# Optimization experiments

Hardware: AMD Instinct MI355X
Metric: run time of the kernel (lower is better)

## Reference

```python
import jax, jax.numpy as jnp
import numpy as np
from jax import lax

N, EMB, AED, H, KCL = 4096, 768, 512, 8, 32
HD = AED // H
TEMP, THR, EPS, MAX_IT = 0.5, 1e-4, 1e-6, 100


def setup_inputs() -> dict:
    key = jax.random.key(0)
    ks = jax.random.split(key, 9)
    s = 0.02
    return {
        "embeddings": jax.random.normal(ks[0], (N, EMB), jnp.float32),
        "qw": jax.random.normal(ks[1], (EMB, AED), jnp.float32) * s,
        "kw": jax.random.normal(ks[2], (EMB, AED), jnp.float32) * s,
        "vw": jax.random.normal(ks[3], (EMB, AED), jnp.float32) * s,
        "in_proj_w": jax.random.normal(ks[4], (3 * AED, AED), jnp.float32) * s,
        "in_proj_b": jnp.zeros((3 * AED,), jnp.float32),
        "out_w": jax.random.normal(ks[5], (AED, AED), jnp.float32) * s,
        "out_b": jnp.zeros((AED,), jnp.float32),
        "init_idx": jax.random.randint(ks[6], (KCL,), 0, N, dtype=jnp.int32),
    }


def _mha(q, k, v, Wi, bi, Wo, bo):
    # torch nn.MultiheadAttention, batch_first, batch==1, no mask
    Wq, Wk, Wv = jnp.split(Wi, 3, axis=0)
    bq, bk, bv = jnp.split(bi, 3)
    n = q.shape[0]
    qh = (q @ Wq.T + bq).reshape(n, H, HD).transpose(1, 0, 2)  # [H,N,hd]
    kh = (k @ Wk.T + bk).reshape(n, H, HD).transpose(1, 0, 2)
    vh = (v @ Wv.T + bv).reshape(n, H, HD).transpose(1, 0, 2)
    scores = jnp.einsum("hqd,hkd->hqk", qh, kh) / jnp.sqrt(jnp.float32(HD))
    attn = jax.nn.softmax(scores, axis=-1)            # [H,N,N]
    o = jnp.einsum("hqk,hkd->hqd", attn, vh)          # [H,N,hd]
    o = o.transpose(1, 0, 2).reshape(n, AED)
    return o @ Wo.T + bo


def _cdist(X, C):
    # euclidean distance [N,K]
    d2 = (jnp.sum(X * X, 1)[:, None] + jnp.sum(C * C, 1)[None, :]
          - 2.0 * (X @ C.T))
    return jnp.sqrt(jnp.maximum(d2, 0.0))


def _dkm_step(X, C):
    a = jax.nn.softmax(-_cdist(X, C) / TEMP, axis=1)  # [N,K]
    a_sum = jnp.sum(a, axis=0) + EPS                  # [K]
    C_new = (a.T @ X) / a_sum[:, None]                # [K,E]
    return a, C_new


def _dkm(X, C_init):
    a, C_new = _dkm_step(X, C_init)
    diff = jnp.sum(jnp.abs(C_new - C_init))
    def body(carry, _):
        C, a, C_new, diff = carry
        cont = diff > THR
        C2 = jnp.where(cont, C_new, C)
        a2, C_new2 = _dkm_step(X, C2)
        a2 = jnp.where(cont, a2, a)
        C_new2 = jnp.where(cont, C_new2, C_new)
        diff2 = jnp.where(cont, jnp.sum(jnp.abs(C_new2 - C2)), diff)
        return (C2, a2, C_new2, diff2), None
    (C, a, _, _), _ = lax.scan(body, (C_init, a, C_new, diff), None, length=MAX_IT)
    return C, a


def reference(embeddings, qw, kw, vw, in_proj_w, in_proj_b, out_w, out_b, init_idx):
    q = embeddings @ qw
    k = embeddings @ kw
    v = embeddings @ vw
    tr = _mha(q, k, v, in_proj_w, in_proj_b, out_w, out_b)  # [N,AED]
    init_c = lax.stop_gradient(tr[init_idx])                # detached init
    C, a = _dkm(tr, init_c)
    return C, a
```

## Files before the change

### kernel.cpp

```cpp
#include <hip/hip_runtime.h>
#include <hip/hip_bf16.h>


typedef __hip_bfloat16 bf16;
typedef __attribute__((ext_vector_type(8))) short s16x8;
typedef __attribute__((ext_vector_type(4))) float f32x4;

__device__ __forceinline__ void  stv(float* p, float v) { *p = v; }
__device__ __forceinline__ void  stv(bf16*  p, float v) { *p = __float2bfloat16(v); }

__device__ __forceinline__ float gload(const float* p)
{
    return __hip_atomic_load(p, __ATOMIC_RELAXED, __HIP_MEMORY_SCOPE_AGENT);
}
__device__ __forceinline__ void gstore(float* p, float v)
{
    __hip_atomic_store(p, v, __ATOMIC_RELAXED, __HIP_MEMORY_SCOPE_AGENT);
}
__device__ __forceinline__ void gstore2(float2* p, float2 v)
{
    unsigned long long u; __builtin_memcpy(&u, &v, 8);
    __hip_atomic_store((unsigned long long*)p, u, __ATOMIC_RELAXED, __HIP_MEMORY_SCOPE_AGENT);
}

__device__ __forceinline__ unsigned bf16word(float v)
{
    bf16 b = __float2bfloat16(v);
    unsigned short u;
    __builtin_memcpy(&u, &b, 2);
    return ((unsigned)u) << 16;
}

__device__ __forceinline__ void stage8(const float* g, bf16* d)
{
    const float4 a = *(const float4*)g;
    const float4 b = *(const float4*)(g + 4);
    union { uint4 u; bf16 h[8]; } r;
    r.h[0] = __float2bfloat16(a.x); r.h[1] = __float2bfloat16(a.y);
    r.h[2] = __float2bfloat16(a.z); r.h[3] = __float2bfloat16(a.w);
    r.h[4] = __float2bfloat16(b.x); r.h[5] = __float2bfloat16(b.y);
    r.h[6] = __float2bfloat16(b.z); r.h[7] = __float2bfloat16(b.w);
    *(uint4*)d = r.u;
}
__device__ __forceinline__ void stage8(const bf16* g, bf16* d)
{
    *(uint4*)d = *(const uint4*)g;
}
__device__ __forceinline__ void load8f(const float* g, float* v)
{
    const float4 a = *(const float4*)g; const float4 b = *(const float4*)(g + 4);
    v[0]=a.x; v[1]=a.y; v[2]=a.z; v[3]=a.w; v[4]=b.x; v[5]=b.y; v[6]=b.z; v[7]=b.w;
}
__device__ __forceinline__ void load8f(const bf16* g, float* v)
{
    union { uint4 u; bf16 h[8]; } r; r.u = *(const uint4*)g;
#pragma unroll
    for (int j = 0; j < 8; j++) v[j] = __bfloat162float(r.h[j]);
}

struct P3 { const void* a[3]; const void* b[3]; const float* bi[3]; void* c[3]; };

template<typename TA, typename TB, typename TC, bool BT, bool BIAS>
__global__ __launch_bounds__(256) void mgemm(P3 p, int M, int N, int K)
{
    __shared__ __align__(16) bf16 As[64][40];
    __shared__ __align__(16) bf16 Bs[64][40];
    const int z = blockIdx.z;
    const TA* A = (const TA*)p.a[z];
    const TB* B = (const TB*)p.b[z];
    const float* bias = p.bi[z];
    TC* C = (TC*)p.c[z];
    const int m0 = blockIdx.x * 64, n0 = blockIdx.y * 64;
    const int t = threadIdx.x;
    const int w = t >> 6, lane = t & 63, quad = lane >> 4, l15 = lane & 15;
    f32x4 acc[4];
#pragma unroll
    for (int i = 0; i < 4; i++) acc[i] = (f32x4){0.f, 0.f, 0.f, 0.f};
    for (int k0 = 0; k0 < K; k0 += 32) {
        {
            int r = t >> 2, c = (t & 3) * 8;
            stage8(&A[(size_t)(m0 + r) * K + k0 + c], &As[r][c]);
        }
        if constexpr (BT) {
            int r = t >> 2, c = (t & 3) * 8;
            stage8(&B[(size_t)(n0 + r) * K + k0 + c], &Bs[r][c]);
        } else {
            int k = t >> 3, n8 = (t & 7) * 8;
            float v[8];
            load8f(&B[(size_t)(k0 + k) * N + n0 + n8], v);
#pragma unroll
            for (int j = 0; j < 8; j++) Bs[n8 + j][k] = __float2bfloat16(v[j]);
        }
        __syncthreads();
        s16x8 af = *(const s16x8*)&As[w * 16 + l15][quad * 8];
#pragma unroll
        for (int nt = 0; nt < 4; nt++) {
            s16x8 bfv = *(const s16x8*)&Bs[nt * 16 + l15][quad * 8];
            acc[nt] = __builtin_amdgcn_mfma_f32_16x16x32_bf16(af, bfv, acc[nt], 0, 0, 0);
        }
        __syncthreads();
    }
#pragma unroll
    for (int nt = 0; nt < 4; nt++) {
        int col = n0 + nt * 16 + l15;
        float bv = 0.f;
        if constexpr (BIAS) bv = bias[col];
#pragma unroll
        for (int r = 0; r < 4; r++) {
            int row = m0 + w * 16 + quad * 4 + r;
            stv(&C[(size_t)row * N + col], acc[nt][r] + bv);
        }
    }
}

__global__ __launch_bounds__(256) void attn_mfma(
    const bf16* __restrict__ qh, const bf16* __restrict__ kh,
    const bf16* __restrict__ vh, bf16* __restrict__ oatt)
{
    __shared__ __align__(16) bf16  Qs[64][72];
    __shared__ __align__(16) bf16  Ks[2][64][72];
    __shared__ __align__(16) bf16  Vt[2][64][72];
    __shared__ __align__(16) float Ss[64][68];
    __shared__ __align__(16) bf16  Ps[64][72];
    __shared__ float mrow[64], lrow[64], arow[64];
    const int bid = blockIdx.x;
    const int h = bid & 7, q0 = (bid >> 3) * 64;
    const int t = threadIdx.x;
    const int w = t >> 6, lane = t & 63, quad = lane >> 4, l15 = lane & 15;

#pragma unroll
    for (int i = 0; i < 2; i++) {
        int idx = t + i * 256;
        int r = idx >> 3, c = (idx & 7) * 8;
        *(uint4*)&Qs[r][c] = *(const uint4*)&qh[(size_t)(q0 + r) * 512 + h * 64 + c];
    }
    if (t < 64) { mrow[t] = -1e30f; lrow[t] = 0.f; }
    f32x4 accO[4];
#pragma unroll
    for (int i = 0; i < 4; i++) accO[i] = (f32x4){0.f, 0.f, 0.f, 0.f};

    const int sidx0 = t, sidx1 = t + 256;
    const int sr0 = sidx0 >> 3, sc0 = (sidx0 & 7) * 8;
    const int sr1 = sidx1 >> 3, sc1v = (sidx1 & 7) * 8;
    uint4 kreg0 = *(const uint4*)&kh[(size_t)sr0 * 512 + h * 64 + sc0];
    uint4 vreg0 = *(const uint4*)&vh[(size_t)sr0 * 512 + h * 64 + sc0];
    uint4 kreg1 = *(const uint4*)&kh[(size_t)sr1 * 512 + h * 64 + sc1v];
    uint4 vreg1 = *(const uint4*)&vh[(size_t)sr1 * 512 + h * 64 + sc1v];
    {
        *(uint4*)&Ks[0][sr0][sc0] = kreg0;
        union { uint4 u; bf16 b[8]; } vv; vv.u = vreg0;
        int rlo = sr0 & 7, rch = sr0 >> 3, rx = sidx0 & 7;
#pragma unroll
        for (int j = 0; j < 8; j++)
            Vt[0][sc0 + j][rlo | (((rch ^ rx) & 7) << 3)] = vv.b[j];
    }
    {
        *(uint4*)&Ks[0][sr1][sc1v] = kreg1;
        union { uint4 u; bf16 b[8]; } vv; vv.u = vreg1;
        int rlo = sr1 & 7, rch = sr1 >> 3, rx = sidx1 & 7;
#pragma unroll
        for (int j = 0; j < 8; j++)
            Vt[0][sc1v + j][rlo | (((rch ^ rx) & 7) << 3)] = vv.b[j];
    }
    {
        size_t base0 = (size_t)(64 + sr0) * 512 + h * 64;
        size_t base1 = (size_t)(64 + sr1) * 512 + h * 64;
        kreg0 = *(const uint4*)&kh[base0 + sc0];
        vreg0 = *(const uint4*)&vh[base0 + sc0];
        kreg1 = *(const uint4*)&kh[base1 + sc1v];
        vreg1 = *(const uint4*)&vh[base1 + sc1v];
    }
    __syncthreads();

    for (int s = 0; s < 64; s++) {
        const int cur = s & 1;
        if (s + 1 < 64) {
            const int nxt = cur ^ 1;
            {
                *(uint4*)&Ks[nxt][sr0][sc0] = kreg0;
                union { uint4 u; bf16 b[8]; } vv; vv.u = vreg0;
                int rlo = sr0 & 7, rch = sr0 >> 3, rx = sidx0 & 7;
#pragma unroll
                for (int j = 0; j < 8; j++)
                    Vt[nxt][sc0 + j][rlo | (((rch ^ rx) & 7) << 3)] = vv.b[j];
            }
            {
                *(uint4*)&Ks[nxt][sr1][sc1v] = kreg1;
                union { uint4 u; bf16 b[8]; } vv; vv.u = vreg1;
                int rlo = sr1 & 7, rch = sr1 >> 3, rx = sidx1 & 7;
#pragma unroll
                for (int j = 0; j < 8; j++)
                    Vt[nxt][sc1v + j][rlo | (((rch ^ rx) & 7) << 3)] = vv.b[j];
            }
            if (s + 2 < 64) {
                size_t base0 = (size_t)((s + 2) * 64 + sr0) * 512 + h * 64;
                size_t base1 = (size_t)((s + 2) * 64 + sr1) * 512 + h * 64;
                kreg0 = *(const uint4*)&kh[base0 + sc0];
                vreg0 = *(const uint4*)&vh[base0 + sc0];
                kreg1 = *(const uint4*)&kh[base1 + sc1v];
                vreg1 = *(const uint4*)&vh[base1 + sc1v];
            }
        }
        f32x4 accS[4];
#pragma unroll
        for (int i = 0; i < 4; i++) accS[i] = (f32x4){0.f, 0.f, 0.f, 0.f};
        __builtin_amdgcn_s_setprio(1);
#pragma unroll
        for (int dc = 0; dc < 64; dc += 32) {
            s16x8 aq = *(const s16x8*)&Qs[w * 16 + l15][dc + quad * 8];
#pragma unroll
            for (int nt = 0; nt < 4; nt++) {
                s16x8 bk = *(const s16x8*)&Ks[cur][nt * 16 + l15][dc + quad * 8];
                accS[nt] = __builtin_amdgcn_mfma_f32_16x16x32_bf16(aq, bk, accS[nt], 0, 0, 0);
            }
        }
        __builtin_amdgcn_s_setprio(0);
#pragma unroll
        for (int nt = 0; nt < 4; nt++)
#pragma unroll
            for (int r = 0; r < 4; r++)
                Ss[w * 16 + quad * 4 + r][nt * 16 + l15] = accS[nt][r] * 0.1803368801f;
        {
            const int srow = t >> 2, sseg = t & 3;
            float* sp = &Ss[srow][sseg * 16];
            float4 s0 = *(const float4*)(sp + 0);
            float4 s1 = *(const float4*)(sp + 4);
            float4 s2 = *(const float4*)(sp + 8);
            float4 s3 = *(const float4*)(sp + 12);
            float mold = mrow[srow];
            float m01 = fmaxf(fmaxf(s0.x, s0.y), fmaxf(s0.z, s0.w));
            float m23 = fmaxf(fmaxf(s1.x, s1.y), fmaxf(s1.z, s1.w));
            float m45 = fmaxf(fmaxf(s2.x, s2.y), fmaxf(s2.z, s2.w));
            float m67 = fmaxf(fmaxf(s3.x, s3.y), fmaxf(s3.z, s3.w));
            float mx = fmaxf(fmaxf(m01, m23), fmaxf(m45, m67));
            mx = fmaxf(mx, mold);
            mx = fmaxf(mx, __shfl_xor(mx, 1));
            mx = fmaxf(mx, __shfl_xor(mx, 2));
            s0.x = exp2f(s0.x - mx); s0.y = exp2f(s0.y - mx);
            s0.z = exp2f(s0.z - mx); s0.w = exp2f(s0.w - mx);
            s1.x = exp2f(s1.x - mx); s1.y = exp2f(s1.y - mx);
            s1.z = exp2f(s1.z - mx); s1.w = exp2f(s1.w - mx);
            s2.x = exp2f(s2.x - mx); s2.y = exp2f(s2.y - mx);
            s2.z = exp2f(s2.z - mx); s2.w = exp2f(s2.w - mx);
            s3.x = exp2f(s3.x - mx); s3.y = exp2f(s3.y - mx);
            s3.z = exp2f(s3.z - mx); s3.w = exp2f(s3.w - mx);
            union { uint4 u; bf16 h[8]; } pa, pb;
            pa.h[0] = __float2bfloat16(s0.x); pa.h[1] = __float2bfloat16(s0.y);
            pa.h[2] = __float2bfloat16(s0.z); pa.h[3] = __float2bfloat16(s0.w);
            pa.h[4] = __float2bfloat16(s1.x); pa.h[5] = __float2bfloat16(s1.y);
            pa.h[6] = __float2bfloat16(s1.z); pa.h[7] = __float2bfloat16(s1.w);
            pb.h[0] = __float2bfloat16(s2.x); pb.h[1] = __float2bfloat16(s2.y);
            pb.h[2] = __float2bfloat16(s2.z); pb.h[3] = __float2bfloat16(s2.w);
            pb.h[4] = __float2bfloat16(s3.x); pb.h[5] = __float2bfloat16(s3.y);
            pb.h[6] = __float2bfloat16(s3.z); pb.h[7] = __float2bfloat16(s3.w);
            *(uint4*)&Ps[srow][sseg * 16]     = pa.u;
            *(uint4*)&Ps[srow][sseg * 16 + 8] = pb.u;
            float ps = (s0.x + s0.y + s0.z + s0.w) + (s1.x + s1.y + s1.z + s1.w)
                     + (s2.x + s2.y + s2.z + s2.w) + (s3.x + s3.y + s3.z + s3.w);
            ps += __shfl_xor(ps, 1);
            ps += __shfl_xor(ps, 2);
            if (sseg == 0) {
                float al = exp2f(mold - mx);
                lrow[srow] = lrow[srow] * al + ps;
                mrow[srow] = mx;
                arow[srow] = al;
            }
        }
        float al4[4];
#pragma unroll
        for (int r = 0; r < 4; r++) al4[r] = arow[w * 16 + quad * 4 + r];
#pragma unroll
        for (int dt = 0; dt < 4; dt++)
#pragma unroll
            for (int r = 0; r < 4; r++) accO[dt][r] *= al4[r];
        __builtin_amdgcn_s_setprio(1);
#pragma unroll
        for (int kc = 0; kc < 64; kc += 32) {
            s16x8 pf = *(const s16x8*)&Ps[w * 16 + l15][kc + quad * 8];
#pragma unroll
            for (int dt = 0; dt < 4; dt++) {
                int vrow = dt * 16 + l15;
                s16x8 bv = *(const s16x8*)&Vt[cur][vrow][((((kc >> 3) + quad) ^ (vrow >> 3)) & 7) << 3];
                accO[dt] = __builtin_amdgcn_mfma_f32_16x16x32_bf16(pf, bv, accO[dt], 0, 0, 0);
            }
        }
        __builtin_amdgcn_s_setprio(0);
        __syncthreads();
    }
#pragma unroll
    for (int dt = 0; dt < 4; dt++)
#pragma unroll
        for (int r = 0; r < 4; r++) {
            int row = w * 16 + quad * 4 + r;
            oatt[(size_t)(q0 + row) * 512 + h * 64 + dt * 16 + l15] =
                __float2bfloat16(accO[dt][r] / lrow[row]);
        }
}

__global__ __launch_bounds__(64) void k_bar_init(unsigned* bar, unsigned* gen)
{
    if (threadIdx.x < 9) bar[threadIdx.x] = 0u;
    if (threadIdx.x == 0) *gen = 0u;
}

__device__ __forceinline__ unsigned gridbar_f(unsigned* bar, unsigned* gen,
                                              const float* dptr, float thr,
                                              unsigned* bcast)
{
    __syncthreads();
    if (threadIdx.x == 0) {
        unsigned g = __hip_atomic_load(gen, __ATOMIC_RELAXED, __HIP_MEMORY_SCOPE_AGENT);
        const int sub = blockIdx.x & 7;
        unsigned newg = 0;
        bool released = false;
        if (__hip_atomic_fetch_add(&bar[sub], 1u, __ATOMIC_RELAXED, __HIP_MEMORY_SCOPE_AGENT) == 15u) {
            __hip_atomic_store(&bar[sub], 0u, __ATOMIC_RELAXED, __HIP_MEMORY_SCOPE_AGENT);
            asm volatile("s_waitcnt vmcnt(0)" ::: "memory");
            if (__hip_atomic_fetch_add(&bar[8], 1u, __ATOMIC_RELAXED, __HIP_MEMORY_SCOPE_AGENT) == 7u) {
                __hip_atomic_store(&bar[8], 0u, __ATOMIC_RELAXED, __HIP_MEMORY_SCOPE_AGENT);
                unsigned flag = 0u;
                if (dptr) flag = (gload(dptr) > thr) ? 1u : 0u;
                asm volatile("s_waitcnt vmcnt(0)" ::: "memory");
                newg = (((g >> 1) + 1u) << 1) | flag;
                __hip_atomic_store(gen, newg, __ATOMIC_RELAXED, __HIP_MEMORY_SCOPE_AGENT);
                released = true;
            }
        }
        if (!released) {
            unsigned ng;
            do {
                ng = __hip_atomic_load(gen, __ATOMIC_RELAXED, __HIP_MEMORY_SCOPE_AGENT);
                if ((ng >> 1) != (g >> 1)) break;
                __builtin_amdgcn_s_sleep(1);
            } while (true);
            newg = ng;
        }
        *bcast = newg;
    }
    __syncthreads();
    return *bcast & 1u;
}

__global__ __launch_bounds__(256) void dkm_persist(
    const float* __restrict__ X, const int* __restrict__ idxp,
    float* __restrict__ Cacc, float* __restrict__ Cb0, float* __restrict__ Cb1,
    float* __restrict__ asumb, float* __restrict__ diffb, float* __restrict__ cnormb,
    unsigned* bar, unsigned* gen, unsigned* __restrict__ out)
{
    const int b = blockIdx.x, t = threadIdx.x;
    const int n0 = b * 32;
    __shared__ float Cs[128][32];
    __shared__ float as_[32][32];
    __shared__ float red[256];
    __shared__ float xn[32];
    __shared__ unsigned gw;

    {
        int rl = t >> 3, j = t & 7;
        const float* p = X + (size_t)(n0 + rl) * 512 + j * 64;
        float s = 0.f;
#pragma unroll
        for (int i = 0; i < 64; i++) { float v = p[i]; s += v * v; }
        as_[rl][j] = s;
        __syncthreads();
        if (t < 32) {
            float tot = 0.f;
#pragma unroll
            for (int jj = 0; jj < 8; jj++) tot += as_[t][jj];
            xn[t] = tot;
        }
        if (t < 128) {
            int o = b * 128 + t;
            gstore(&Cb0[o], X[(size_t)idxp[o & 31] * 512 + (o >> 5)]);
        }
        int z = b * 256 + t;
        if (z < 3072) gstore(&asumb[z], 0.f);
        if (z < 97)   gstore(&diffb[z], 0.f);
        if (z < 3136) gstore(&cnormb[z], 0.f);
    }
    gridbar_f(bar, gen, nullptr, 0.f, &gw);
    if (b < 32) {
        float s = 0.f;
        for (int e = t; e < 512; e += 256) { float v = gload(&Cb0[e * 32 + b]); s += v * v; }
        red[t] = s; __syncthreads();
        for (int st = 128; st > 0; st >>= 1) { if (t < st) red[t] += red[t + st]; __syncthreads(); }
        if (t == 0) gstore(&cnormb[b], red[0]);
    }
    gridbar_f(bar, gen, nullptr, 0.f, &gw);

    const int k = t & 31, rg = t >> 5;
    int ifin = 96;
    float pre[16];
#pragma unroll
    for (int j = 0; j < 16; j++) pre[j] = gload(&Cb0[t + j * 256]);
    for (int i = 0; i <= 96; i++) {
        const float* Cc = (i & 1) ? Cb1 : Cb0;
        float* Cn = (i & 1) ? Cb0 : Cb1;
        float dots[4] = {0.f, 0.f, 0.f, 0.f};
        for (int ec = 0; ec < 4; ec++) {
            __syncthreads();
#pragma unroll
            for (int j = 0; j < 16; j++) {
                int idx = t + j * 256;
                Cs[idx >> 5][idx & 31] = pre[j];
            }
            __syncthreads();
            if (ec < 3) {
#pragma unroll
                for (int j = 0; j < 16; j++)
                    pre[j] = gload(&Cc[(ec + 1) * 4096 + t + j * 256]);
            }
            const float* xb = X + (size_t)(n0 + rg) * 512 + ec * 128;
#pragma unroll 4
            for (int ee4 = 0; ee4 < 128; ee4 += 4) {
                float4 x0 = *(const float4*)&xb[ee4];
                float4 x1 = *(const float4*)&xb[8 * 512 + ee4];
                float4 x2 = *(const float4*)&xb[16 * 512 + ee4];
                float4 x3 = *(const float4*)&xb[24 * 512 + ee4];
                {
                    float cv = Cs[ee4 + 0][k];
                    dots[0] += x0.x * cv; dots[1] += x1.x * cv;
                    dots[2] += x2.x * cv; dots[3] += x3.x * cv;
                }
                {
                    float cv = Cs[ee4 + 1][k];
                    dots[0] += x0.y * cv; dots[1] += x1.y * cv;
                    dots[2] += x2.y * cv; dots[3] += x3.y * cv;
                }
                {
                    float cv = Cs[ee4 + 2][k];
                    dots[0] += x0.z * cv; dots[1] += x1.z * cv;
                    dots[2] += x2.z * cv; dots[3] += x3.z * cv;
                }
                {
                    float cv = Cs[ee4 + 3][k];
                    dots[0] += x0.w * cv; dots[1] += x1.w * cv;
                    dots[2] += x2.w * cv; dots[3] += x3.w * cv;
                }
            }
        }
        float cn = gload(&cnormb[i * 32 + k]);
#pragma unroll
        for (int rr = 0; rr < 4; rr++) {
            int rl = rg + rr * 8;
            float d2 = xn[rl] + cn - 2.f * dots[rr];
            as_[rl][k] = -2.f * sqrtf(fmaxf(d2, 0.f));
        }
        __syncthreads();
        if (t < 32) {
            float mx = -1e30f;
            for (int kk = 0; kk < 32; kk++) mx = fmaxf(mx, as_[t][kk]);
            float su = 0.f;
            for (int kk = 0; kk < 32; kk++) su += expf(as_[t][kk] - mx);
            float inv = 1.f / su;
            for (int kk = 0; kk < 32; kk++) as_[t][kk] = expf(as_[t][kk] - mx) * inv;
        }
        __syncthreads();
        if (i == 96) {
#pragma unroll
            for (int i2 = 0; i2 < 4; i2++) {
                int o = t + i2 * 256;
                int r = o >> 5, kk = o & 31;
                out[16384 + (n0 + r) * 32 + kk] = bf16word(as_[r][kk]);
            }
            break;
        }
        if (t < 32) {
            float s = 0.f;
            for (int r = 0; r < 32; r++) s += as_[r][t];
            atomicAdd(&asumb[i * 32 + t], s);
        }
        {
            float acc[64];
#pragma unroll
            for (int i2 = 0; i2 < 64; i2++) acc[i2] = 0.f;
            const float2* X2 = (const float2*)(X + (size_t)n0 * 512);
            for (int r = 0; r < 32; r++) {
                float2 xv = X2[r * 256 + t];
                const float4* ar4 = (const float4*)as_[r];
#pragma unroll
                for (int kq = 0; kq < 8; kq++) {
                    float4 av = ar4[kq];
                    acc[(kq * 4 + 0) * 2 + 0] += av.x * xv.x; acc[(kq * 4 + 0) * 2 + 1] += av.x * xv.y;
                    acc[(kq * 4 + 1) * 2 + 0] += av.y * xv.x; acc[(kq * 4 + 1) * 2 + 1] += av.y * xv.y;
                    acc[(kq * 4 + 2) * 2 + 0] += av.z * xv.x; acc[(kq * 4 + 2) * 2 + 1] += av.z * xv.y;
                    acc[(kq * 4 + 3) * 2 + 0] += av.w * xv.x; acc[(kq * 4 + 3) * 2 + 1] += av.w * xv.y;
                }
            }
            float2* cb = (float2*)(Cacc + (size_t)b * 16384);
#pragma unroll
            for (int k2 = 0; k2 < 32; k2++) {
                float2 wv; wv.x = acc[k2 * 2 + 0]; wv.y = acc[k2 * 2 + 1];
                gstore2(&cb[k2 * 256 + t], wv);
            }
        }
        gridbar_f(bar, gen, nullptr, 0.f, &gw);
        {
            const int j = t & 127, half = t >> 7;
            const int o = b * 128 + j;
            float s = 0.f;
            for (int p = half * 64; p < half * 64 + 64; p++) s += gload(&Cacc[(size_t)p * 16384 + o]);
            red[t] = s;
            __syncthreads();
            float df = 0.f, cp = 0.f;
            if (t < 128) {
                float tot = red[t] + red[t + 128];
                int kk = o >> 9, e = o & 511;
                float cn2 = tot / (gload(&asumb[i * 32 + kk]) + 1e-6f);
                gstore(&Cn[e * 32 + kk], cn2);
                df = fabsf(cn2 - gload(&Cc[e * 32 + kk]));
                cp = cn2 * cn2;
            }
            __syncthreads();
            red[t] = df; __syncthreads();
            for (int st = 128; st > 0; st >>= 1) { if (t < st) red[t] += red[t + st]; __syncthreads(); }
            if (t == 0) atomicAdd(&diffb[i], red[0]);
            __syncthreads();
            red[t] = cp; __syncthreads();
            for (int st = 128; st > 0; st >>= 1) { if (t < st) red[t] += red[t + st]; __syncthreads(); }
            if (t == 0) atomicAdd(&cnormb[(i + 1) * 32 + (b >> 2)], red[0]);
        }
        unsigned cont = gridbar_f(bar, gen, &diffb[i], 1e-4f, &gw);
        if (!cont) {
            ifin = i;
#pragma unroll
            for (int i2 = 0; i2 < 4; i2++) {
                int o = t + i2 * 256;
                int r = o >> 5, kk = o & 31;
                out[16384 + (n0 + r) * 32 + kk] = bf16word(as_[r][kk]);
            }
            break;
        }
#pragma unroll
        for (int j = 0; j < 16; j++) pre[j] = gload(&Cn[t + j * 256]);
    }
    {
        const float* Cf = (ifin & 1) ? Cb1 : Cb0;
        if (t < 128) {
            int idx = b * 128 + t;
            int kk = idx >> 9, e = idx & 511;
            out[idx] = bf16word(gload(&Cf[e * 32 + kk]));
        }
    }
}

extern "C" void kernel_launch(void* const* d_in, const int* in_sizes, int n_in,
                              void* d_out, int out_size, void* d_ws, size_t ws_size,
                              hipStream_t stream)
{
    const size_t NEED = 25323292;
    if (ws_size < NEED) return;

    const float* emb = (const float*)d_in[0];
    const float* qw  = (const float*)d_in[1];
    const float* kw  = (const float*)d_in[2];
    const float* vw  = (const float*)d_in[3];
    const float* ipw = (const float*)d_in[4];
    const float* ipb = (const float*)d_in[5];
    const float* ow  = (const float*)d_in[6];
    const float* ob  = (const float*)d_in[7];
    const int*   idx = (const int*)d_in[8];
    unsigned* out = (unsigned*)d_out;

    float* ws    = (float*)d_ws;
    bf16*  qkv   = (bf16*)ws;
    bf16*  weff  = (bf16*)(ws + 3145728);
    bf16*  oatt  = (bf16*)(ws + 3145728);
    float* X     = ws;
    float* Cacc  = ws + 4194304;
    float* Cb0   = ws + 6291456;
    float* Cb1   = ws + 6307840;
    float* asumb = ws + 6324224;
    float* diffb = ws + 6327456;
    float* cnormb= ws + 6327557;
    unsigned* bar = (unsigned*)(ws + 6324224 + 3072);
    unsigned* gen = (unsigned*)(ws + 6330822);

    bf16* qh = qkv;
    bf16* kh = qkv + 2097152;
    bf16* vh = qkv + 4194304;

    k_bar_init<<<1, 64, 0, stream>>>(bar, gen);

    P3 pw;
    pw.a[0] = qw;  pw.a[1] = kw;  pw.a[2] = vw;
    pw.b[0] = ipw; pw.b[1] = ipw + 262144; pw.b[2] = ipw + 524288;
    pw.bi[0] = pw.bi[1] = pw.bi[2] = nullptr;
    pw.c[0] = weff; pw.c[1] = weff + 393216; pw.c[2] = weff + 786432;
    mgemm<float, float, bf16, true, false><<<dim3(12, 8, 3), 256, 0, stream>>>(pw, 768, 512, 512);

    P3 pq;
    pq.a[0] = pq.a[1] = pq.a[2] = emb;
    pq.b[0] = weff; pq.b[1] = weff + 393216; pq.b[2] = weff + 786432;
    pq.bi[0] = ipb; pq.bi[1] = ipb + 512; pq.bi[2] = ipb + 1024;
    pq.c[0] = qh; pq.c[1] = kh; pq.c[2] = vh;
    mgemm<float, bf16, bf16, false, true><<<dim3(64, 8, 3), 256, 0, stream>>>(pq, 4096, 512, 768);

    attn_mfma<<<dim3(512), 256, 0, stream>>>(qh, kh, vh, oatt);

    P3 pt;
    pt.a[0] = oatt; pt.b[0] = ow; pt.bi[0] = ob; pt.c[0] = X;
    pt.a[1] = pt.a[2] = pt.b[1] = pt.b[2] = nullptr;
    pt.bi[1] = pt.bi[2] = nullptr; pt.c[1] = pt.c[2] = nullptr;
    mgemm<bf16, float, float, true, true><<<dim3(64, 8, 1), 256, 0, stream>>>(pt, 4096, 512, 512);

    dkm_persist<<<dim3(128), 256, 0, stream>>>(X, idx, Cacc, Cb0, Cb1,
                                               asumb, diffb, cnormb, bar, gen, out);
}
```

Baseline: 450.8 us.

## Software-pipeline QK^T MFMA one tile ahead of softmax in attention loop

```diff
diff --git a/kernel.cpp b/kernel.cpp
--- a/kernel.cpp
+++ b/kernel.cpp
@@ -171,11 +171,26 @@
         vreg1 = *(const uint4*)&vh[base1 + sc1v];
     }
     __syncthreads();
+    f32x4 accA[4], accB[4];
+    {
+#pragma unroll
+        for (int i = 0; i < 4; i++) accA[i] = (f32x4){0.f, 0.f, 0.f, 0.f};
+        __builtin_amdgcn_s_setprio(1);
+#pragma unroll
+        for (int dc = 0; dc < 64; dc += 32) {
+            s16x8 aq = *(const s16x8*)&Qs[w * 16 + l15][dc + quad * 8];
+#pragma unroll
+            for (int nt = 0; nt < 4; nt++) {
+                s16x8 bk = *(const s16x8*)&Ks[0][nt * 16 + l15][dc + quad * 8];
+                accA[nt] = __builtin_amdgcn_mfma_f32_16x16x32_bf16(aq, bk, accA[nt], 0, 0, 0);
+            }
+        }
+        __builtin_amdgcn_s_setprio(0);
+    }
 
     for (int s = 0; s < 64; s++) {
-        const int cur = s & 1;
+        const int cur = s & 1, nxt = cur ^ 1;
         if (s + 1 < 64) {
-            const int nxt = cur ^ 1;
             {
                 *(uint4*)&Ks[nxt][sr0][sc0] = kreg0;
                 union { uint4 u; bf16 b[8]; } vv; vv.u = vreg0;
@@ -201,25 +216,27 @@
                 vreg1 = *(const uint4*)&vh[base1 + sc1v];
             }
         }
-        f32x4 accS[4];
-#pragma unroll
-        for (int i = 0; i < 4; i++) accS[i] = (f32x4){0.f, 0.f, 0.f, 0.f};
-        __builtin_amdgcn_s_setprio(1);
-#pragma unroll
-        for (int dc = 0; dc < 64; dc += 32) {
-            s16x8 aq = *(const s16x8*)&Qs[w * 16 + l15][dc + quad * 8];
-#pragma unroll
-            for (int nt = 0; nt < 4; nt++) {
-                s16x8 bk = *(const s16x8*)&Ks[cur][nt * 16 + l15][dc + quad * 8];
-                accS[nt] = __builtin_amdgcn_mfma_f32_16x16x32_bf16(aq, bk, accS[nt], 0, 0, 0);
-            }
-        }
-        __builtin_amdgcn_s_setprio(0);
+        __syncthreads();
+        if (s + 1 < 64) {
+#pragma unroll
+            for (int i = 0; i < 4; i++) accB[i] = (f32x4){0.f, 0.f, 0.f, 0.f};
+            __builtin_amdgcn_s_setprio(1);
+#pragma unroll
+            for (int dc = 0; dc < 64; dc += 32) {
+                s16x8 aq = *(const s16x8*)&Qs[w * 16 + l15][dc + quad * 8];
+#pragma unroll
+                for (int nt = 0; nt < 4; nt++) {
+                    s16x8 bk = *(const s16x8*)&Ks[nxt][nt * 16 + l15][dc + quad * 8];
+                    accB[nt] = __builtin_amdgcn_mfma_f32_16x16x32_bf16(aq, bk, accB[nt], 0, 0, 0);
+                }
+            }
+            __builtin_amdgcn_s_setprio(0);
+        }
 #pragma unroll
         for (int nt = 0; nt < 4; nt++)
 #pragma unroll
             for (int r = 0; r < 4; r++)
-                Ss[w * 16 + quad * 4 + r][nt * 16 + l15] = accS[nt][r] * 0.1803368801f;
+                Ss[w * 16 + quad * 4 + r][nt * 16 + l15] = accA[nt][r] * 0.1803368801f;
         {
             const int srow = t >> 2, sseg = t & 3;
             float* sp = &Ss[srow][sseg * 16];
@@ -286,6 +303,8 @@
         }
         __builtin_amdgcn_s_setprio(0);
         __syncthreads();
+#pragma unroll
+        for (int i = 0; i < 4; i++) accA[i] = accB[i];
     }
 #pragma unroll
     for (int dt = 0; dt < 4; dt++)
```

Result: no change. 453.8 us (median of 2 runs) (+0.7%).
